# Optimization experiments

Hardware: AMD Instinct MI355X
Metric: run time of the kernel (lower is better)

Reference implementation:

```python
import jax, jax.numpy as jnp
import numpy as np

B, N, IN_F, OUT_F = 8, 2048, 256, 256
ALPHA = 0.2  # LeakyReLU negative slope
NEG_INF = -1e9


def setup_inputs() -> dict:
    key = jax.random.key(0)
    ks = jax.random.split(key, 8)
    h = jax.random.normal(ks[0], (B, N, IN_F), dtype=jnp.float32)
    adj = jax.random.randint(ks[1], (B, N, N), 0, 2, dtype=jnp.int32)
    # xavier-ish scaled params
    W_w = jax.random.normal(ks[2], (OUT_F, IN_F), dtype=jnp.float32) * (1.414 / np.sqrt(IN_F + OUT_F))
    W_b = jnp.zeros((OUT_F,), dtype=jnp.float32)
    ai_w = jax.random.normal(ks[3], (1, OUT_F), dtype=jnp.float32) * (1.414 / np.sqrt(OUT_F + 1))
    ai_b = jnp.zeros((1,), dtype=jnp.float32)
    aj_w = jax.random.normal(ks[4], (1, OUT_F), dtype=jnp.float32) * (1.414 / np.sqrt(OUT_F + 1))
    aj_b = jnp.zeros((1,), dtype=jnp.float32)
    return {"h": h, "adj": adj, "W_w": W_w, "W_b": W_b,
            "ai_w": ai_w, "ai_b": ai_b, "aj_w": aj_w, "aj_b": aj_b}


def reference(h, adj, W_w, W_b, ai_w, ai_b, aj_w, aj_b):
    # Wh: [B, N, F]
    Wh = jnp.einsum('bni,oi->bno', h, W_w) + W_b
    # additive attention scores (pos_embed_dim == 1 so the .view is a transpose)
    Wh1 = jnp.einsum('bnf,of->bno', Wh, ai_w) + ai_b        # [B, N, 1]
    Wh2 = jnp.einsum('bnf,of->bno', Wh, aj_w) + aj_b        # [B, N, 1]
    e = Wh1 + jnp.swapaxes(Wh2, 1, 2)                       # [B, N, N]
    e = jnp.where(e >= 0, e, ALPHA * e)                     # LeakyReLU
    attention = jnp.where(adj > 0, e, NEG_INF)
    attention = jax.nn.softmax(attention, axis=2)
    # dropout: inference mode (training=False) -> identity
    h_hat = jnp.einsum('bnm,bmf->bnf', attention, Wh)
    return jax.nn.elu(h_hat)  # concat=True
```

## Files before the change

### kernel.cpp

```cpp
#include <hip/hip_runtime.h>

typedef __bf16 bf16;
typedef _Float16 f16;
typedef __bf16 bf16x8 __attribute__((ext_vector_type(8)));
typedef _Float16 f16x8 __attribute__((ext_vector_type(8)));
typedef float  f32x4  __attribute__((ext_vector_type(4)));

#define B_  8
#define N_  2048
#define F_  256
#define NTOK (B_ * N_)
static constexpr float LOG2E = 1.44269504088896f;

__device__ __forceinline__ int detect_bf16(const void* h) {
    const unsigned* hw = (const unsigned*)h;
    unsigned w = hw[threadIdx.x & 63];
    unsigned ex = (w >> 7) & 0xFFu;
    unsigned long long b = __ballot(ex > 100u && ex < 150u);
    return __popcll(b) >= 40;
}

__device__ __forceinline__ float ldf(const void* p, int i, int isb) {
    return isb ? (float)((const bf16*)p)[i] : ((const float*)p)[i];
}

__device__ __forceinline__ bf16x8 cvt8(const float* p) {
    float4 a = *(const float4*)p;
    float4 b = *(const float4*)(p + 4);
    bf16x8 r;
    r[0]=(bf16)a.x; r[1]=(bf16)a.y; r[2]=(bf16)a.z; r[3]=(bf16)a.w;
    r[4]=(bf16)b.x; r[5]=(bf16)b.y; r[6]=(bf16)b.z; r[7]=(bf16)b.w;
    return r;
}

__device__ __forceinline__ size_t wht2_idx(int b, int f, int n) {
    int jc = n >> 6;
    int slot = ((n >> 3) & 7) ^ (f & 7);
    return (((size_t)(b * 32 + jc) * F_ + f) << 6) + (slot << 3) + (n & 7);
}

__global__ __launch_bounds__(256)
void k_wht(const void* __restrict__ hv, const void* __restrict__ Wv,
           const void* __restrict__ Wbv, const void* __restrict__ ai_wv,
           const void* __restrict__ ai_bv, const void* __restrict__ aj_wv,
           const void* __restrict__ aj_bv, bf16* __restrict__ WhT2,
           unsigned* __restrict__ adjw) {
    int isb = detect_bf16(hv);
    int ttile = blockIdx.x;
    int fg = threadIdx.x >> 6;
    int lane = threadIdx.x & 63;
    int T0 = ttile * 16;
    int m = lane & 15, quad = lane >> 4;

    f32x4 acc[4];
#pragma unroll
    for (int ft = 0; ft < 4; ++ft) acc[ft] = (f32x4){0.f, 0.f, 0.f, 0.f};

    if (isb) {
        const bf16* hp = (const bf16*)hv + (size_t)(T0 + m) * F_ + quad * 8;
        const bf16* wp = (const bf16*)Wv + (size_t)(fg * 64 + m) * F_ + quad * 8;
#pragma unroll
        for (int kk = 0; kk < F_; kk += 32) {
            bf16x8 hf = *(const bf16x8*)(hp + kk);
#pragma unroll
            for (int ft = 0; ft < 4; ++ft) {
                bf16x8 wf = *(const bf16x8*)(wp + (size_t)ft * 16 * F_ + kk);
                acc[ft] = __builtin_amdgcn_mfma_f32_16x16x32_bf16(wf, hf, acc[ft], 0, 0, 0);
            }
        }
    } else {
        const float* hp = (const float*)hv + (size_t)(T0 + m) * F_ + quad * 8;
        const float* wp = (const float*)Wv + (size_t)(fg * 64 + m) * F_ + quad * 8;
#pragma unroll
        for (int kk = 0; kk < F_; kk += 32) {
            bf16x8 hf = cvt8(hp + kk);
#pragma unroll
            for (int ft = 0; ft < 4; ++ft) {
                bf16x8 wf = cvt8(wp + (size_t)ft * 16 * F_ + kk);
                acc[ft] = __builtin_amdgcn_mfma_f32_16x16x32_bf16(wf, hf, acc[ft], 0, 0, 0);
            }
        }
    }
    int token = T0 + m;
    int b = token >> 11, n = token & (N_ - 1);
    float s_p = 0.f, t_p = 0.f;
#pragma unroll
    for (int ft = 0; ft < 4; ++ft)
#pragma unroll
        for (int r = 0; r < 4; ++r) {
            int f = fg * 64 + ft * 16 + quad * 4 + r;
            float v = acc[ft][r] + ldf(Wbv, f, isb);
            bf16 vb = (bf16)v;
            WhT2[wht2_idx(b, f, n)] = vb;
            float vr = (float)vb;
            s_p += vr * ldf(ai_wv, f, isb);
            t_p += vr * ldf(aj_wv, f, isb);
        }
    s_p += __shfl_down(s_p, 32, 64); s_p += __shfl_down(s_p, 16, 64);
    t_p += __shfl_down(t_p, 32, 64); t_p += __shfl_down(t_p, 16, 64);
    __shared__ float sred[4][16], tred[4][16];
    if (lane < 16) { sred[fg][lane] = s_p; tred[fg][lane] = t_p; }
    __syncthreads();
    if (threadIdx.x < 16) {
        int tid = threadIdx.x;
        int tok = T0 + tid;
        float ss = (sred[0][tid] + sred[1][tid] + sred[2][tid] + sred[3][tid]
                    + ldf(ai_bv, 0, isb)) * LOG2E;
        float tt = (tred[0][tid] + tred[1][tid] + tred[2][tid] + tred[3][tid]
                    + ldf(aj_bv, 0, isb)) * LOG2E;
        f16 th = (f16)tt, sh = (f16)ss;
        unsigned short tu, su;
        __builtin_memcpy(&tu, &th, 2);
        __builtin_memcpy(&su, &sh, 2);
        unsigned w0 = adjw[tok];
        adjw[tok] = (w0 & 0xFFFFu) | ((unsigned)tu << 16);
        unsigned w1 = adjw[NTOK + tok];
        adjw[NTOK + tok] = (w1 & 0xFFFFu) | ((unsigned)su << 16);
    }
}

__device__ __forceinline__ unsigned char pbits(uint4 a, uint4 b) {
    return (unsigned char)((a.x & 1u) | ((a.y & 1u) << 1) | ((a.z & 1u) << 2) |
                           ((a.w & 1u) << 3) | ((b.x & 1u) << 4) |
                           ((b.y & 1u) << 5) | ((b.z & 1u) << 6) |
                           ((b.w & 1u) << 7));
}

__device__ __forceinline__ void stageB(const bf16* tile, char* dst,
                                       int w, int lane) {
#pragma unroll
    for (int r = 0; r < 8; ++r) {
        int off = (w * 8 + r) * 1024;
        const bf16* g = tile + off / 2 + lane * 8;
        __builtin_amdgcn_global_load_lds(
            (const __attribute__((address_space(1))) unsigned*)g,
            (__attribute__((address_space(3))) unsigned*)(dst + off),
            16, 0, 0);
    }
}

__global__ __launch_bounds__(256)
void k_attn(const unsigned* __restrict__ adjw, const bf16* __restrict__ WhT2,
            const void* __restrict__ hv, void* __restrict__ outv) {
    int isb = detect_bf16(hv);
    int bid = blockIdx.x;
    int b = bid >> 6, itile = bid & 63, i0 = itile * 32;
    int tid = threadIdx.x;
    int w = tid >> 6, lane = tid & 63, m = lane & 15, q = lane >> 4;
    int mt = w >> 1, jh = w & 1;

    __shared__ __align__(16) char smem[70656];
    char* Bbuf0 = smem;
    char* Bbuf1 = smem + 32768;
    f16* tLDS   = (f16*)(smem + 65536);
    unsigned char* pack0 = (unsigned char*)(smem + 69632);
    unsigned char* pack1 = (unsigned char*)(smem + 69888);
    float* red  = (float*)smem;

    const bf16* batch_tiles = WhT2 + ((size_t)b * 32) * F_ * 64;

#pragma unroll
    for (int k = 0; k < 8; ++k) {
        int idx = k * 256 + tid;
        unsigned wv = adjw[b * N_ + idx];
        unsigned short us = (unsigned short)(wv >> 16);
        f16 tv; __builtin_memcpy(&tv, &us, 2);
        tLDS[idx] = tv;
    }
    int row = i0 + mt * 16 + m;
    unsigned swd = adjw[NTOK + b * N_ + row];
    unsigned short su = (unsigned short)(swd >> 16);
    f16 sh; __builtin_memcpy(&sh, &su, 2);
    float s2i = (float)sh;

    int prow = tid >> 3, ps = tid & 7;
    const unsigned* arow = adjw + ((size_t)(b * N_ + i0 + prow)) * N_ + ps * 8;
    {
        uint4 x0 = *(const uint4*)arow, x1 = *(const uint4*)(arow + 4);
        pack0[prow * 8 + ps] = pbits(x0, x1);
    }
    stageB(batch_tiles, Bbuf0, w, lane);
    __syncthreads();

    bf16x8 ones;
#pragma unroll
    for (int k = 0; k < 8; ++k) ones[k] = (bf16)1.0f;

    f32x4 acc[16];
#pragma unroll
    for (int ft = 0; ft < 16; ++ft) acc[ft] = (f32x4){0.f, 0.f, 0.f, 0.f};
    f32x4 acc_l = {0.f, 0.f, 0.f, 0.f};

    for (int c = 0; c < 32; ++c) {
        char* Bcur = (c & 1) ? Bbuf1 : Bbuf0;
        unsigned char* pcur = (c & 1) ? pack1 : pack0;
        uint4 aw0, aw1;
        bool pre = (c < 31);
        if (pre) {
            stageB(batch_tiles + (size_t)(c + 1) * F_ * 64,
                   (c & 1) ? Bbuf0 : Bbuf1, w, lane);
            aw0 = *(const uint4*)(arow + (size_t)(c + 1) * 64);
            aw1 = *(const uint4*)(arow + (size_t)(c + 1) * 64 + 4);
        }
        unsigned long long pb64 =
            *(const unsigned long long*)(pcur + (mt * 16 + m) * 8);
        unsigned bits8 = (unsigned)(pb64 >> ((jh * 4 + q) * 8)) & 0xFFu;
        f16x8 tv = *(const f16x8*)(tLDS + c * 64 + jh * 32 + q * 8);

        bf16x8 af;
#pragma unroll
        for (int qq = 0; qq < 8; ++qq) {
            float x = s2i + (float)tv[qq];
            x = fmaxf(x, 0.2f * x);
            float pv = ((bits8 >> qq) & 1u) ? __builtin_amdgcn_exp2f(x) : 0.f;
            af[qq] = (bf16)pv;
        }
        int sbase = (jh * 4 + q);
#pragma unroll
        for (int ft = 0; ft < 16; ++ft) {
            int fr = ft * 16 + m;
            int psl = sbase ^ (m & 7);
            bf16x8 bfr = *(const bf16x8*)(Bcur + fr * 128 + psl * 16);
            acc[ft] = __builtin_amdgcn_mfma_f32_16x16x32_bf16(af, bfr, acc[ft], 0, 0, 0);
        }
        acc_l = __builtin_amdgcn_mfma_f32_16x16x32_bf16(af, ones, acc_l, 0, 0, 0);
        if (pre)
            ((c & 1) ? pack0 : pack1)[prow * 8 + ps] = pbits(aw0, aw1);
        __syncthreads();
    }

    if (jh == 1) {
#pragma unroll
        for (int r = 0; r < 4; ++r) {
            int rr = mt * 16 + q * 4 + r;
#pragma unroll
            for (int ft = 0; ft < 16; ++ft)
                red[rr * 257 + ft * 16 + m] = acc[ft][r];
            if (m == 0) red[rr * 257 + 256] = acc_l[r];
        }
    }
    __syncthreads();
    if (jh == 0) {
#pragma unroll
        for (int r = 0; r < 4; ++r) {
            int rr = mt * 16 + q * 4 + r;
            float lf = acc_l[r] + red[rr * 257 + 256];
            float rl = (lf > 0.f) ? (1.f / lf) : 0.f;
            size_t ob = ((size_t)b * N_ + i0 + rr) * F_;
#pragma unroll
            for (int ft = 0; ft < 16; ++ft) {
                int f = ft * 16 + m;
                float v = acc[ft][r] + red[rr * 257 + f];
                v *= rl;
                v = (v > 0.f) ? v : (__builtin_amdgcn_exp2f(v * LOG2E) - 1.f);
                if (isb) ((bf16*)outv)[ob + f] = (bf16)v;
                else     ((float*)outv)[ob + f] = v;
            }
        }
    }
}

extern "C" void kernel_launch(void* const* d_in, const int* in_sizes, int n_in,
                              void* d_out, int out_size, void* d_ws, size_t ws_size,
                              hipStream_t stream) {
    (void)in_sizes; (void)n_in; (void)out_size; (void)ws_size;
    const void* h    = d_in[0];
    unsigned*   adjw = (unsigned*)d_in[1];
    const void* W_w  = d_in[2];
    const void* W_b  = d_in[3];
    const void* ai_w = d_in[4];
    const void* ai_b = d_in[5];
    const void* aj_w = d_in[6];
    const void* aj_b = d_in[7];

    bf16* WhT2 = (bf16*)d_ws;

    k_wht <<<dim3(1024), dim3(256), 0, stream>>>(h, W_w, W_b, ai_w, ai_b,
                                                 aj_w, aj_b, WhT2, adjw);
    k_attn<<<dim3(512),  dim3(256), 0, stream>>>(adjw, WhT2, h, d_out);
}
```

Measured before the change: 272.0 us.

## Load Wh fragments directly from global in MFMA order, drop LDS staging

Re-lays out the transposed Wh buffer so that each lane's MFMA B-fragment is a contiguous 16-byte chunk, and has the attention kernel read it straight from global memory instead of staging through double-buffered LDS. Each lane now loads its own adjacency bits directly rather than through a shared packed-bit buffer. This removes the per-chunk barriers, cuts LDS use so three blocks can fit per CU, and reorders block IDs so concurrent blocks span batches. The cost is that every wave issues its own global/L2 reads of Wh with no LDS reuse, so latency hiding now depends on occupancy and cache hits.

```diff
diff --git a/kernel.cpp b/kernel.cpp
--- a/kernel.cpp
+++ b/kernel.cpp
@@ -34,9 +34,9 @@
 }
 
 __device__ __forceinline__ size_t wht2_idx(int b, int f, int n) {
-    int jc = n >> 6;
-    int slot = ((n >> 3) & 7) ^ (f & 7);
-    return (((size_t)(b * 32 + jc) * F_ + f) << 6) + (slot << 3) + (n & 7);
+    int jc = n >> 6, jh = (n >> 5) & 1, jq = (n >> 3) & 3, jl = n & 7;
+    return ((((size_t)(b * 32 + jc) * 16 + (f >> 4)) * 2 + jh) * 4 + jq) * 128
+           + (size_t)(f & 15) * 8 + jl;
 }
 
 __global__ __launch_bounds__(256)
@@ -126,38 +126,19 @@
                            ((b.w & 1u) << 7));
 }
 
-__device__ __forceinline__ void stageB(const bf16* tile, char* dst,
-                                       int w, int lane) {
-#pragma unroll
-    for (int r = 0; r < 8; ++r) {
-        int off = (w * 8 + r) * 1024;
-        const bf16* g = tile + off / 2 + lane * 8;
-        __builtin_amdgcn_global_load_lds(
-            (const __attribute__((address_space(1))) unsigned*)g,
-            (__attribute__((address_space(3))) unsigned*)(dst + off),
-            16, 0, 0);
-    }
-}
-
-__global__ __launch_bounds__(256)
+__global__ __launch_bounds__(256, 3)
 void k_attn(const unsigned* __restrict__ adjw, const bf16* __restrict__ WhT2,
             const void* __restrict__ hv, void* __restrict__ outv) {
     int isb = detect_bf16(hv);
     int bid = blockIdx.x;
-    int b = bid >> 6, itile = bid & 63, i0 = itile * 32;
+    int b = bid & 7, itile = bid >> 3, i0 = itile * 32;
     int tid = threadIdx.x;
     int w = tid >> 6, lane = tid & 63, m = lane & 15, q = lane >> 4;
     int mt = w >> 1, jh = w & 1;
 
-    __shared__ __align__(16) char smem[70656];
-    char* Bbuf0 = smem;
-    char* Bbuf1 = smem + 32768;
-    f16* tLDS   = (f16*)(smem + 65536);
-    unsigned char* pack0 = (unsigned char*)(smem + 69632);
-    unsigned char* pack1 = (unsigned char*)(smem + 69888);
-    float* red  = (float*)smem;
-
-    const bf16* batch_tiles = WhT2 + ((size_t)b * 32) * F_ * 64;
+    __shared__ __align__(16) char smem[33024];
+    f16* tLDS  = (f16*)smem;
+    float* red = (float*)smem;
 
 #pragma unroll
     for (int k = 0; k < 8; ++k) {
@@ -172,15 +153,11 @@
     unsigned short su = (unsigned short)(swd >> 16);
     f16 sh; __builtin_memcpy(&sh, &su, 2);
     float s2i = (float)sh;
-
-    int prow = tid >> 3, ps = tid & 7;
-    const unsigned* arow = adjw + ((size_t)(b * N_ + i0 + prow)) * N_ + ps * 8;
-    {
-        uint4 x0 = *(const uint4*)arow, x1 = *(const uint4*)(arow + 4);
-        pack0[prow * 8 + ps] = pbits(x0, x1);
-    }
-    stageB(batch_tiles, Bbuf0, w, lane);
-    __syncthreads();
+    __syncthreads();
+
+    const unsigned* arow = adjw + ((size_t)(b * N_ + row)) * N_ + jh * 32 + q * 8;
+    const char* bbase = (const char*)WhT2 + ((size_t)b * 32) * 32768
+                        + jh * 1024 + lane * 16;
 
     bf16x8 ones;
 #pragma unroll
@@ -191,20 +168,15 @@
     for (int ft = 0; ft < 16; ++ft) acc[ft] = (f32x4){0.f, 0.f, 0.f, 0.f};
     f32x4 acc_l = {0.f, 0.f, 0.f, 0.f};
 
+    uint4 awA = *(const uint4*)(arow);
+    uint4 awB = *(const uint4*)(arow + 4);
+
     for (int c = 0; c < 32; ++c) {
-        char* Bcur = (c & 1) ? Bbuf1 : Bbuf0;
-        unsigned char* pcur = (c & 1) ? pack1 : pack0;
-        uint4 aw0, aw1;
-        bool pre = (c < 31);
-        if (pre) {
-            stageB(batch_tiles + (size_t)(c + 1) * F_ * 64,
-                   (c & 1) ? Bbuf0 : Bbuf1, w, lane);
-            aw0 = *(const uint4*)(arow + (size_t)(c + 1) * 64);
-            aw1 = *(const uint4*)(arow + (size_t)(c + 1) * 64 + 4);
-        }
-        unsigned long long pb64 =
-            *(const unsigned long long*)(pcur + (mt * 16 + m) * 8);
-        unsigned bits8 = (unsigned)(pb64 >> ((jh * 4 + q) * 8)) & 0xFFu;
+        unsigned bits8 = (unsigned)pbits(awA, awB);
+        if (c < 31) {
+            awA = *(const uint4*)(arow + (size_t)(c + 1) * 64);
+            awB = *(const uint4*)(arow + (size_t)(c + 1) * 64 + 4);
+        }
         f16x8 tv = *(const f16x8*)(tLDS + c * 64 + jh * 32 + q * 8);
 
         bf16x8 af;
@@ -215,19 +187,17 @@
             float pv = ((bits8 >> qq) & 1u) ? __builtin_amdgcn_exp2f(x) : 0.f;
             af[qq] = (bf16)pv;
         }
-        int sbase = (jh * 4 + q);
+
+        const char* bp = bbase + (size_t)c * 32768;
 #pragma unroll
         for (int ft = 0; ft < 16; ++ft) {
-            int fr = ft * 16 + m;
-            int psl = sbase ^ (m & 7);
-            bf16x8 bfr = *(const bf16x8*)(Bcur + fr * 128 + psl * 16);
+            bf16x8 bfr = *(const bf16x8*)(bp + ft * 2048);
             acc[ft] = __builtin_amdgcn_mfma_f32_16x16x32_bf16(af, bfr, acc[ft], 0, 0, 0);
         }
         acc_l = __builtin_amdgcn_mfma_f32_16x16x32_bf16(af, ones, acc_l, 0, 0, 0);
-        if (pre)
-            ((c & 1) ? pack0 : pack1)[prow * 8 + ps] = pbits(aw0, aw1);
-        __syncthreads();
-    }
+    }
+
+    __syncthreads();
 
     if (jh == 1) {
 #pragma unroll
```

New measurement: 365.4 us. 1.34x slower.

## Pre-convert h and W to bf16 in separate kernel; interleave batches across attention blocks

Applied to the files above, without the earlier changes.

Adds a conversion kernel that writes bf16 copies of h and W into workspace, so the projection kernel reads bf16 directly. Before, every block re-read and re-converted the fp32 W rows. This adds one extra launch and a round trip of h through memory. The attention kernel's block-to-batch mapping also changes so consecutive blocks cover different batches, which changes L2 locality and load balance.

```diff
diff --git a/kernel.cpp b/kernel.cpp
--- a/kernel.cpp
+++ b/kernel.cpp
@@ -10,6 +10,8 @@
 #define N_  2048
 #define F_  256
 #define NTOK (B_ * N_)
+#define NH   (NTOK * F_)
+#define NW   (F_ * F_)
 static constexpr float LOG2E = 1.44269504088896f;
 
 __device__ __forceinline__ int detect_bf16(const void* h) {
@@ -24,15 +26,6 @@
     return isb ? (float)((const bf16*)p)[i] : ((const float*)p)[i];
 }
 
-__device__ __forceinline__ bf16x8 cvt8(const float* p) {
-    float4 a = *(const float4*)p;
-    float4 b = *(const float4*)(p + 4);
-    bf16x8 r;
-    r[0]=(bf16)a.x; r[1]=(bf16)a.y; r[2]=(bf16)a.z; r[3]=(bf16)a.w;
-    r[4]=(bf16)b.x; r[5]=(bf16)b.y; r[6]=(bf16)b.z; r[7]=(bf16)b.w;
-    return r;
-}
-
 __device__ __forceinline__ size_t wht2_idx(int b, int f, int n) {
     int jc = n >> 6;
     int slot = ((n >> 3) & 7) ^ (f & 7);
@@ -40,12 +33,40 @@
 }
 
 __global__ __launch_bounds__(256)
+void k_cvt(const void* __restrict__ hv, const void* __restrict__ Wv,
+           bf16* __restrict__ hb, bf16* __restrict__ Wb) {
+    if (detect_bf16(hv)) return;
+    size_t base = ((size_t)blockIdx.x * 256 + threadIdx.x) * 8;
+    {
+        const float* src = (const float*)hv + base;
+        float4 a = *(const float4*)src;
+        float4 b = *(const float4*)(src + 4);
+        bf16x8 r;
+        r[0]=(bf16)a.x; r[1]=(bf16)a.y; r[2]=(bf16)a.z; r[3]=(bf16)a.w;
+        r[4]=(bf16)b.x; r[5]=(bf16)b.y; r[6]=(bf16)b.z; r[7]=(bf16)b.w;
+        *(bf16x8*)(hb + base) = r;
+    }
+    if (base < NW) {
+        const float* src = (const float*)Wv + base;
+        float4 a = *(const float4*)src;
+        float4 b = *(const float4*)(src + 4);
+        bf16x8 r;
+        r[0]=(bf16)a.x; r[1]=(bf16)a.y; r[2]=(bf16)a.z; r[3]=(bf16)a.w;
+        r[4]=(bf16)b.x; r[5]=(bf16)b.y; r[6]=(bf16)b.z; r[7]=(bf16)b.w;
+        *(bf16x8*)(Wb + base) = r;
+    }
+}
+
+__global__ __launch_bounds__(256)
 void k_wht(const void* __restrict__ hv, const void* __restrict__ Wv,
+           const bf16* __restrict__ hcv, const bf16* __restrict__ Wcv,
            const void* __restrict__ Wbv, const void* __restrict__ ai_wv,
            const void* __restrict__ ai_bv, const void* __restrict__ aj_wv,
            const void* __restrict__ aj_bv, bf16* __restrict__ WhT2,
            unsigned* __restrict__ adjw) {
     int isb = detect_bf16(hv);
+    const bf16* hb = isb ? (const bf16*)hv : hcv;
+    const bf16* Wb = isb ? (const bf16*)Wv : Wcv;
     int ttile = blockIdx.x;
     int fg = threadIdx.x >> 6;
     int lane = threadIdx.x & 63;
@@ -56,29 +77,15 @@
 #pragma unroll
     for (int ft = 0; ft < 4; ++ft) acc[ft] = (f32x4){0.f, 0.f, 0.f, 0.f};
 
-    if (isb) {
-        const bf16* hp = (const bf16*)hv + (size_t)(T0 + m) * F_ + quad * 8;
-        const bf16* wp = (const bf16*)Wv + (size_t)(fg * 64 + m) * F_ + quad * 8;
-#pragma unroll
-        for (int kk = 0; kk < F_; kk += 32) {
-            bf16x8 hf = *(const bf16x8*)(hp + kk);
-#pragma unroll
-            for (int ft = 0; ft < 4; ++ft) {
-                bf16x8 wf = *(const bf16x8*)(wp + (size_t)ft * 16 * F_ + kk);
-                acc[ft] = __builtin_amdgcn_mfma_f32_16x16x32_bf16(wf, hf, acc[ft], 0, 0, 0);
-            }
-        }
-    } else {
-        const float* hp = (const float*)hv + (size_t)(T0 + m) * F_ + quad * 8;
-        const float* wp = (const float*)Wv + (size_t)(fg * 64 + m) * F_ + quad * 8;
-#pragma unroll
-        for (int kk = 0; kk < F_; kk += 32) {
-            bf16x8 hf = cvt8(hp + kk);
-#pragma unroll
-            for (int ft = 0; ft < 4; ++ft) {
-                bf16x8 wf = cvt8(wp + (size_t)ft * 16 * F_ + kk);
-                acc[ft] = __builtin_amdgcn_mfma_f32_16x16x32_bf16(wf, hf, acc[ft], 0, 0, 0);
-            }
+    const bf16* hp = hb + (size_t)(T0 + m) * F_ + quad * 8;
+    const bf16* wp = Wb + (size_t)(fg * 64 + m) * F_ + quad * 8;
+#pragma unroll
+    for (int kk = 0; kk < F_; kk += 32) {
+        bf16x8 hf = *(const bf16x8*)(hp + kk);
+#pragma unroll
+        for (int ft = 0; ft < 4; ++ft) {
+            bf16x8 wf = *(const bf16x8*)(wp + (size_t)ft * 16 * F_ + kk);
+            acc[ft] = __builtin_amdgcn_mfma_f32_16x16x32_bf16(wf, hf, acc[ft], 0, 0, 0);
         }
     }
     int token = T0 + m;
@@ -144,7 +151,7 @@
             const void* __restrict__ hv, void* __restrict__ outv) {
     int isb = detect_bf16(hv);
     int bid = blockIdx.x;
-    int b = bid >> 6, itile = bid & 63, i0 = itile * 32;
+    int b = bid & 7, itile = bid >> 3, i0 = itile * 32;
     int tid = threadIdx.x;
     int w = tid >> 6, lane = tid & 63, m = lane & 15, q = lane >> 4;
     int mt = w >> 1, jh = w & 1;
@@ -274,8 +281,12 @@
     const void* aj_b = d_in[7];
 
     bf16* WhT2 = (bf16*)d_ws;
-
-    k_wht <<<dim3(1024), dim3(256), 0, stream>>>(h, W_w, W_b, ai_w, ai_b,
-                                                 aj_w, aj_b, WhT2, adjw);
+    bf16* hcv  = (bf16*)((char*)d_ws + (8  << 20));
+    bf16* Wcv  = (bf16*)((char*)d_ws + (16 << 20));
+
+    k_cvt <<<dim3(2048), dim3(256), 0, stream>>>(h, W_w, hcv, Wcv);
+    k_wht <<<dim3(1024), dim3(256), 0, stream>>>(h, W_w, hcv, Wcv, W_b,
+                                                 ai_w, ai_b, aj_w, aj_b,
+                                                 WhT2, adjw);
     k_attn<<<dim3(512),  dim3(256), 0, stream>>>(adjw, WhT2, h, d_out);
 }
```

After: 262.4 us. 3.5% less time.
